# Kernel optimization log

Hardware: AMD Instinct MI355X
Metric: run time of the kernel (lower is better)

Reference implementation:

```python
import jax, jax.numpy as jnp
import numpy as np

N = 100000       # nodes
E = 3200000      # edges (avg degree 32)
NFEAT, NHID, NCLASS = 256, 128, 40


def setup_inputs() -> dict:
    key = jax.random.key(0)
    ks = jax.random.split(key, 6)
    x = jax.random.normal(ks[0], (N, NFEAT), jnp.float32)
    edge_rows = jax.random.randint(ks[1], (E,), 0, N)   # destination nodes
    edge_cols = jax.random.randint(ks[2], (E,), 0, N)   # source nodes
    # SageConv proj: Linear(2*in, out, bias=False); weight stored [out, in] torch-style
    W1 = jax.random.normal(ks[3], (NHID, 2 * NFEAT), jnp.float32) * 0.05
    W2 = jax.random.normal(ks[4], (NHID, 2 * NHID), jnp.float32) * 0.05
    mlp_W = jax.random.normal(ks[5], (NCLASS, NHID), jnp.float32) * 0.05  # init.normal_(std=0.05)
    mlp_b = jnp.zeros((NCLASS,), jnp.float32)
    return {"x": x, "W1": W1, "W2": W2, "mlp_W": mlp_W, "mlp_b": mlp_b,
            "edge_rows": edge_rows, "edge_cols": edge_cols}


def _sage_conv(h, W, rows, cols, deg):
    # neigh = spmm(adj, h) / (deg + 1); adj binary COO (rows <- cols)
    neigh = jax.ops.segment_sum(h[cols], rows, num_segments=N) / (deg + 1.0)[:, None]
    return jnp.concatenate([h, neigh], axis=-1) @ W.T


def reference(x, W1, W2, mlp_W, mlp_b, edge_rows, edge_cols):
    deg = jax.ops.segment_sum(jnp.ones((E,), x.dtype), edge_rows, num_segments=N)
    h = jax.nn.relu(_sage_conv(x, W1, edge_rows, edge_cols, deg))   # dropout: eval no-op
    h = jax.nn.relu(_sage_conv(h, W2, edge_rows, edge_cols, deg))
    logits = h @ mlp_W.T + mlp_b
    return jax.nn.log_softmax(logits, axis=1)
```

## Files before the change

kernel.cpp:

```cpp
#include <hip/hip_runtime.h>
#include <hip/hip_bf16.h>

#define NFEAT 256
#define NHID  128
#define NCLASS 40

typedef __attribute__((ext_vector_type(8))) short short8;
typedef __attribute__((ext_vector_type(4))) float float4v;

__device__ __forceinline__ unsigned short f2bf(float f) {
    union { float f; unsigned u; } v; v.f = f;
    unsigned r = v.u + 0x7fff + ((v.u >> 16) & 1);
    return (unsigned short)(r >> 16);
}
__device__ __forceinline__ float bflo(unsigned u) { return __uint_as_float(u << 16); }
__device__ __forceinline__ float bfhi(unsigned u) { return __uint_as_float(u & 0xffff0000u); }
__device__ __forceinline__ unsigned cvtpk_bf16(float a, float b) {
    unsigned r;
    asm("v_cvt_pk_bf16_f32 %0, %1, %2" : "=v"(r) : "v"(a), "v"(b));
    return r;
}

__device__ __forceinline__ void ld_g2l16(const unsigned short* gp, unsigned short* lp) {
    __builtin_amdgcn_global_load_lds((const __attribute__((address_space(1))) unsigned short*)gp,
                                     (__attribute__((address_space(3))) unsigned short*)lp,
                                     16, 0, 0);
}

#define TILE_E 4096
#define WCAP   20480


__global__ __launch_bounds__(256) void prep_fused(const int* __restrict__ rows,
                                                  const int* __restrict__ cols,
                                                  int* __restrict__ gcur,
                                                  unsigned* __restrict__ binned, int E, int nbuck,
                                                  int nblk,
                                                  const float* __restrict__ W1,
                                                  const float* __restrict__ W2,
                                                  const float* __restrict__ Wm,
                                                  unsigned short* __restrict__ Wp1,
                                                  unsigned short* __restrict__ Wp2,
                                                  unsigned short* __restrict__ Wb,
                                                  const float* __restrict__ X,
                                                  unsigned short* __restrict__ X16, int N) {
    int t = threadIdx.x;
    if ((int)blockIdx.x >= nblk + 560) {
        int idx0 = (blockIdx.x - nblk - 560) * 2048;
        #pragma unroll
        for (int it = 0; it < 8; ++it) {
            int idx = idx0 + it * 256 + t;
            int r = idx >> 5, u = idx & 31;
            if (r < N) {
                const float4* px = reinterpret_cast<const float4*>(X + (size_t)r * 256 + u * 8);
                float4 v0 = px[0], v1 = px[1];
                uint4 q;
                q.x = cvtpk_bf16(v0.x, v0.y); q.y = cvtpk_bf16(v0.z, v0.w);
                q.z = cvtpk_bf16(v1.x, v1.y); q.w = cvtpk_bf16(v1.z, v1.w);
                *reinterpret_cast<uint4*>(&X16[(size_t)r * 256 + ((u ^ (r & 7)) * 8)]) = q;
            }
        }
        return;
    }
    if ((int)blockIdx.x >= nblk) {
        int b = blockIdx.x - nblk;
        if (b < 256) {
            float v = (b < 128) ? W1[b * 512 + t] : W1[(b - 128) * 512 + 256 + t];
            Wp1[(size_t)(t >> 5) * 8192 + b * 32 + (t & 31)] = f2bf(v);
        } else if (b < 512) {
            int o = b - 256;
            if (t < 128) {
                float v = (o < 128) ? W2[o * 256 + t] : W2[(o - 128) * 256 + 128 + t];
                Wp2[(size_t)(t >> 5) * 8192 + o * 32 + (t & 31)] = f2bf(v);
            }
        } else {
            int o = b - 512;
            if (t < 128) Wb[o * 128 + t] = (o < NCLASS) ? f2bf(Wm[o * 128 + t]) : 0;
        }
        return;
    }
    __shared__ int hh[256];
    __shared__ int lbase[256];
    __shared__ int lcur[256];
    hh[t] = 0;
    __syncthreads();
    int e0 = blockIdx.x * TILE_E;
    int4 rv[4];
    #pragma unroll
    for (int it = 0; it < TILE_E / 1024; ++it) {
        int base = e0 + (it * 256 + t) * 4;
        if (base + 3 < E) {
            rv[it] = *reinterpret_cast<const int4*>(&rows[base]);
            atomicAdd(&hh[rv[it].x >> 9], 1);
            atomicAdd(&hh[rv[it].y >> 9], 1);
            atomicAdd(&hh[rv[it].z >> 9], 1);
            atomicAdd(&hh[rv[it].w >> 9], 1);
        } else {
            for (int k = 0; k < 4; ++k)
                if (base + k < E) atomicAdd(&hh[rows[base + k] >> 9], 1);
        }
    }
    __syncthreads();
    if (t < nbuck) {
        int h = hh[t];
        lbase[t] = t * WCAP + (h ? atomicAdd(&gcur[t], h) : 0);
        lcur[t] = 0;
    }
    __syncthreads();
    #pragma unroll
    for (int it = 0; it < TILE_E / 1024; ++it) {
        int base = e0 + (it * 256 + t) * 4;
        if (base + 3 < E) {
            int4 r = rv[it];
            int4 c = *reinterpret_cast<const int4*>(&cols[base]);
            int b0 = r.x >> 9, b1 = r.y >> 9, b2 = r.z >> 9, b3 = r.w >> 9;
            int d0 = lbase[b0] + atomicAdd(&lcur[b0], 1);
            int d1 = lbase[b1] + atomicAdd(&lcur[b1], 1);
            int d2 = lbase[b2] + atomicAdd(&lcur[b2], 1);
            int d3 = lbase[b3] + atomicAdd(&lcur[b3], 1);
            binned[d0] = ((unsigned)(r.x & 511) << 17) | (unsigned)c.x;
            binned[d1] = ((unsigned)(r.y & 511) << 17) | (unsigned)c.y;
            binned[d2] = ((unsigned)(r.z & 511) << 17) | (unsigned)c.z;
            binned[d3] = ((unsigned)(r.w & 511) << 17) | (unsigned)c.w;
        } else {
            for (int k = 0; k < 4; ++k)
                if (base + k < E) {
                    int r = rows[base + k];
                    int b = r >> 9;
                    int dst = lbase[b] + atomicAdd(&lcur[b], 1);
                    binned[dst] = ((unsigned)(r & 511) << 17) | (unsigned)cols[base + k];
                }
        }
    }
}

__global__ __launch_bounds__(512) void gemm1_fw(const unsigned short* __restrict__ X16,
                                                const unsigned short* __restrict__ Wp,
                                                unsigned short* __restrict__ PS,
                                                unsigned char* __restrict__ PN8,
                                                int M, int nfw,
                                                const unsigned* __restrict__ binned,
                                                const int* __restrict__ gcur,
                                                int4* __restrict__ rpd,
                                                int* __restrict__ csr_cols, int N) {
    __shared__ __align__(16) char smem[65536];
    const int t = threadIdx.x;

    if ((int)blockIdx.x < nfw) {
        int* h    = (int*)smem;
        int* ps   = h + 512;
        int* lcur = ps + 256;
        int w = blockIdx.x;
        int r0 = w << 9;
        h[t] = 0;
        if (t < 256) ps[t] = 0;
        __syncthreads();
        int beg = w * WCAP, end = beg + gcur[w];
        for (int e = beg + t; e < end; e += 512)
            atomicAdd(&h[binned[e] >> 17], 1);
        __syncthreads();
        int pair = 0;
        if (t < 256) { pair = h[2 * t] + h[2 * t + 1]; ps[t] = pair; }
        __syncthreads();
        for (int off = 1; off < 256; off <<= 1) {
            int tmp = (t >= off && t < 256) ? ps[t - off] : 0;
            __syncthreads();
            if (t < 256) ps[t] += tmp;
            __syncthreads();
        }
        if (t < 256) {
            int base0 = beg + ps[t] - pair;
            int base1 = base0 + h[2 * t];
            int r_a = r0 + 2 * t, r_b = r0 + 2 * t + 1;
            if (r_a < N) {
                int4 m; m.x = base0; m.y = h[2 * t];
                m.z = __float_as_int(1.0f / ((float)h[2 * t] + 1.0f)); m.w = 0;
                rpd[r_a] = m;
            }
            if (r_b < N) {
                int4 m; m.x = base1; m.y = h[2 * t + 1];
                m.z = __float_as_int(1.0f / ((float)h[2 * t + 1] + 1.0f)); m.w = 0;
                rpd[r_b] = m;
            }
            lcur[2 * t] = base0;
            lcur[2 * t + 1] = base1;
        }
        __syncthreads();
        for (int e = beg + t; e < end; e += 512) {
            unsigned v = binned[e];
            int idx = atomicAdd(&lcur[v >> 17], 1);
            csr_cols[idx] = (int)(v & 0x1FFFFu);
        }
        return;
    }

    unsigned short* const sA = (unsigned short*)smem;
    const int lane = t & 63;
    const int wave = t >> 6;
    const int m0 = (blockIdx.x - nfw) * 128;
    const int wm = (wave >> 2) * 64;
    const int wn = (wave & 3) * 64;
    const int r15 = lane & 15;
    const int l4  = lane >> 4;

    #pragma unroll
    for (int it = 0; it < 8; ++it) {
        int row = it * 16 + (t >> 5);
        int gm  = min(m0 + row, M - 1);
        ld_g2l16(X16 + (size_t)gm * 256 + (t & 31) * 8,
                 (unsigned short*)(smem + it * 8192 + wave * 1024));
    }
    __syncthreads();

    float4v acc[4][4] = {{{0.f,0.f,0.f,0.f}}};
    #pragma unroll
    for (int k = 0; k < 8; ++k) {
        short8 aF[4], bF[4];
        #pragma unroll
        for (int i = 0; i < 4; ++i) {
            int row  = wm + i * 16 + r15;
            int koct = k * 4 + l4;
            int u    = koct ^ (row & 7);
            aF[i] = *reinterpret_cast<const short8*>(&sA[row * 256 + u * 8]);
        }
        #pragma unroll
        for (int j = 0; j < 4; ++j) {
            int o = wn + j * 16 + r15;
            bF[j] = *reinterpret_cast<const short8*>(&Wp[(size_t)k * 8192 + o * 32 + l4 * 8]);
        }
        #pragma unroll
        for (int i = 0; i < 4; ++i)
            #pragma unroll
            for (int j = 0; j < 4; ++j)
                acc[i][j] = __builtin_amdgcn_mfma_f32_16x16x32_bf16(aF[i], bF[j], acc[i][j], 0, 0, 0);
    }

    #pragma unroll
    for (int i = 0; i < 4; ++i) {
        #pragma unroll
        for (int r = 0; r < 4; ++r) {
            int row = m0 + wm + i * 16 + (lane >> 4) * 4 + r;
            #pragma unroll
            for (int j = 0; j < 4; ++j) {
                float v  = acc[i][j][r];
                float vn = __shfl_xor(v, 1);
                int cN = wn + j * 16 + r15;
                if (row < M && !(r15 & 1)) {
                    if (cN < 128) {
                        *reinterpret_cast<unsigned*>(&PS[(size_t)row * 128 + cN]) = cvtpk_bf16(v, vn);
                    } else {
                        unsigned p8 = __builtin_amdgcn_cvt_pk_fp8_f32(v, vn, 0u, false);
                        *reinterpret_cast<unsigned short*>(&PN8[(size_t)row * 128 + (cN - 128)]) =
                            (unsigned short)p8;
                    }
                }
            }
        }
    }
}

__global__ __launch_bounds__(512) void gemm2_mfma(const unsigned short* __restrict__ H,
                                                  const unsigned short* __restrict__ Wp,
                                                  unsigned short* __restrict__ PS,
                                                  unsigned char* __restrict__ PN8,
                                                  int M) {
    __shared__ __align__(16) unsigned short sA[128 * 128];
    const int t    = threadIdx.x;
    const int lane = t & 63;
    const int wave = t >> 6;
    const int m0 = blockIdx.x * 128;
    const int wm = (wave >> 2) * 64;
    const int wn = (wave & 3) * 64;
    const int r15 = lane & 15;
    const int l4  = lane >> 4;

    #pragma unroll
    for (int it = 0; it < 4; ++it) {
        int row = it * 32 + (t >> 4);
        ld_g2l16(H + (size_t)(m0 + row) * 128 + (t & 15) * 8,
                 (unsigned short*)((char*)sA + it * 8192 + wave * 1024));
    }
    __syncthreads();

    float4v acc[4][4] = {{{0.f,0.f,0.f,0.f}}};
    #pragma unroll
    for (int k = 0; k < 4; ++k) {
        short8 aF[4], bF[4];
        #pragma unroll
        for (int i = 0; i < 4; ++i) {
            int row  = wm + i * 16 + r15;
            int koct = k * 4 + l4;
            int u    = koct ^ (row & 7);
            aF[i] = *reinterpret_cast<const short8*>(&sA[row * 128 + u * 8]);
        }
        #pragma unroll
        for (int j = 0; j < 4; ++j) {
            int o = wn + j * 16 + r15;
            bF[j] = *reinterpret_cast<const short8*>(&Wp[(size_t)k * 8192 + o * 32 + l4 * 8]);
        }
        #pragma unroll
        for (int i = 0; i < 4; ++i)
            #pragma unroll
            for (int j = 0; j < 4; ++j)
                acc[i][j] = __builtin_amdgcn_mfma_f32_16x16x32_bf16(aF[i], bF[j], acc[i][j], 0, 0, 0);
    }

    #pragma unroll
    for (int i = 0; i < 4; ++i) {
        #pragma unroll
        for (int r = 0; r < 4; ++r) {
            int row = m0 + wm + i * 16 + (lane >> 4) * 4 + r;
            #pragma unroll
            for (int j = 0; j < 4; ++j) {
                float v  = acc[i][j][r];
                float vn = __shfl_xor(v, 1);
                int cN = wn + j * 16 + r15;
                if (row < M && !(r15 & 1)) {
                    if (cN < 128) {
                        *reinterpret_cast<unsigned*>(&PS[(size_t)row * 128 + cN]) = cvtpk_bf16(v, vn);
                    } else {
                        unsigned p8 = __builtin_amdgcn_cvt_pk_fp8_f32(v, vn, 0u, false);
                        *reinterpret_cast<unsigned short*>(&PN8[(size_t)row * 128 + (cN - 128)]) =
                            (unsigned short)p8;
                    }
                }
            }
        }
    }
}

__device__ __forceinline__ void acc_fp8x8(uint2 u,
                                          float& a0, float& a1, float& a2, float& a3,
                                          float& a4, float& a5, float& a6, float& a7) {
    auto f01 = __builtin_amdgcn_cvt_pk_f32_fp8(u.x, false);
    auto f23 = __builtin_amdgcn_cvt_pk_f32_fp8(u.x, true);
    auto f45 = __builtin_amdgcn_cvt_pk_f32_fp8(u.y, false);
    auto f67 = __builtin_amdgcn_cvt_pk_f32_fp8(u.y, true);
    a0 += f01[0]; a1 += f01[1]; a2 += f23[0]; a3 += f23[1];
    a4 += f45[0]; a5 += f45[1]; a6 += f67[0]; a7 += f67[1];
}

__global__ __launch_bounds__(256) void gather_combine(const unsigned short* __restrict__ PS,
                                                      const unsigned char* __restrict__ PN8,
                                                      const int4* __restrict__ rpd,
                                                      const int* __restrict__ csr_cols,
                                                      unsigned short* __restrict__ H, int N) {
    int node = (blockIdx.x * blockDim.x + threadIdx.x) >> 6;
    if (node >= N) return;
    int lane = threadIdx.x & 63;
    int grp  = lane >> 4;
    int l16  = lane & 15;
    int4 md = rpd[node];
    int beg = md.x, end = md.x + md.y;
    float id = __int_as_float(md.z);

    uint4 us = {0u, 0u, 0u, 0u};
    if (grp == 0)
        us = *reinterpret_cast<const uint4*>(&PS[(size_t)node * 128 + l16 * 8]);

    float a0=0,a1=0,a2=0,a3=0,a4=0,a5=0,a6=0,a7=0;
    int p0 = beg + grp;
    for (; p0 + 12 < end; p0 += 16) {
        int cA = csr_cols[p0];
        int cB = csr_cols[p0 + 4];
        int cC = csr_cols[p0 + 8];
        int cD = csr_cols[p0 + 12];
        uint2 uA = *reinterpret_cast<const uint2*>(&PN8[(size_t)cA * 128 + l16 * 8]);
        uint2 uB = *reinterpret_cast<const uint2*>(&PN8[(size_t)cB * 128 + l16 * 8]);
        uint2 uC = *reinterpret_cast<const uint2*>(&PN8[(size_t)cC * 128 + l16 * 8]);
        uint2 uD = *reinterpret_cast<const uint2*>(&PN8[(size_t)cD * 128 + l16 * 8]);
        acc_fp8x8(uA, a0, a1, a2, a3, a4, a5, a6, a7);
        acc_fp8x8(uB, a0, a1, a2, a3, a4, a5, a6, a7);
        acc_fp8x8(uC, a0, a1, a2, a3, a4, a5, a6, a7);
        acc_fp8x8(uD, a0, a1, a2, a3, a4, a5, a6, a7);
    }
    for (; p0 < end; p0 += 4) {
        int c = csr_cols[p0];
        uint2 u = *reinterpret_cast<const uint2*>(&PN8[(size_t)c * 128 + l16 * 8]);
        acc_fp8x8(u, a0, a1, a2, a3, a4, a5, a6, a7);
    }
    a0 += __shfl_xor(a0, 16); a1 += __shfl_xor(a1, 16);
    a2 += __shfl_xor(a2, 16); a3 += __shfl_xor(a3, 16);
    a4 += __shfl_xor(a4, 16); a5 += __shfl_xor(a5, 16);
    a6 += __shfl_xor(a6, 16); a7 += __shfl_xor(a7, 16);
    a0 += __shfl_xor(a0, 32); a1 += __shfl_xor(a1, 32);
    a2 += __shfl_xor(a2, 32); a3 += __shfl_xor(a3, 32);
    a4 += __shfl_xor(a4, 32); a5 += __shfl_xor(a5, 32);
    a6 += __shfl_xor(a6, 32); a7 += __shfl_xor(a7, 32);

    if (grp == 0) {
        float h0 = fmaxf(fmaf(a0, id, bflo(us.x)), 0.f);
        float h1 = fmaxf(fmaf(a1, id, bfhi(us.x)), 0.f);
        float h2 = fmaxf(fmaf(a2, id, bflo(us.y)), 0.f);
        float h3 = fmaxf(fmaf(a3, id, bfhi(us.y)), 0.f);
        float h4 = fmaxf(fmaf(a4, id, bflo(us.z)), 0.f);
        float h5 = fmaxf(fmaf(a5, id, bfhi(us.z)), 0.f);
        float h6 = fmaxf(fmaf(a6, id, bflo(us.w)), 0.f);
        float h7 = fmaxf(fmaf(a7, id, bfhi(us.w)), 0.f);
        uint4 o;
        o.x = cvtpk_bf16(h0, h1); o.y = cvtpk_bf16(h2, h3);
        o.z = cvtpk_bf16(h4, h5); o.w = cvtpk_bf16(h6, h7);
        *reinterpret_cast<uint4*>(&H[(size_t)node * 128 + ((l16 ^ (node & 7)) * 8)]) = o;
    }
}

__global__ __launch_bounds__(256) void mlp_head_mfma(const unsigned short* __restrict__ H,
                                                     const unsigned short* __restrict__ Wb,
                                                     const float* __restrict__ bm,
                                                     float* __restrict__ out, int N) {
    __shared__ unsigned short sW[48 * 128];
    int t = threadIdx.x;
    for (int i = t; i < 48 * 128 / 2; i += 256)
        ((unsigned*)sW)[i] = ((const unsigned*)Wb)[i];
    __syncthreads();

    const int wave = t >> 6, lane = t & 63;
    const int m0 = blockIdx.x * 64 + wave * 16;
    if (m0 >= N) return;
    const int r15 = lane & 15;
    const int k8  = (lane >> 4) * 8;
    const int arow = min(m0 + r15, N - 1);

    float4v acc[3] = {{0.f,0.f,0.f,0.f},{0.f,0.f,0.f,0.f},{0.f,0.f,0.f,0.f}};
    #pragma unroll
    for (int k0 = 0; k0 < 128; k0 += 32) {
        int u = (k0 >> 3) + (lane >> 4);
        short8 a = *reinterpret_cast<const short8*>(&H[(size_t)arow * 128 + ((u ^ (arow & 7)) * 8)]);
        #pragma unroll
        for (int f = 0; f < 3; ++f) {
            short8 b = *reinterpret_cast<const short8*>(&sW[(f * 16 + r15) * 128 + k0 + k8]);
            acc[f] = __builtin_amdgcn_mfma_f32_16x16x32_bf16(a, b, acc[f], 0, 0, 0);
        }
    }

    float bias[3]; bool cv[3];
    #pragma unroll
    for (int f = 0; f < 3; ++f) {
        int c = f * 16 + r15;
        cv[f] = (c < NCLASS);
        bias[f] = cv[f] ? bm[c] : 0.f;
    }
    #pragma unroll
    for (int r = 0; r < 4; ++r) {
        int node = m0 + (lane >> 4) * 4 + r;
        float lg[3];
        float m = -1e30f;
        #pragma unroll
        for (int f = 0; f < 3; ++f) {
            lg[f] = cv[f] ? (acc[f][r] + bias[f]) : -1e30f;
            m = fmaxf(m, lg[f]);
        }
        m = fmaxf(m, __shfl_xor(m, 1));
        m = fmaxf(m, __shfl_xor(m, 2));
        m = fmaxf(m, __shfl_xor(m, 4));
        m = fmaxf(m, __shfl_xor(m, 8));
        float s = 0.f;
        #pragma unroll
        for (int f = 0; f < 3; ++f) s += cv[f] ? __expf(lg[f] - m) : 0.f;
        s += __shfl_xor(s, 1);
        s += __shfl_xor(s, 2);
        s += __shfl_xor(s, 4);
        s += __shfl_xor(s, 8);
        float ls = __logf(s);
        if (node < N) {
            #pragma unroll
            for (int f = 0; f < 3; ++f)
                if (cv[f]) out[(size_t)node * NCLASS + f * 16 + r15] = lg[f] - m - ls;
        }
    }
}

extern "C" void kernel_launch(void* const* d_in, const int* in_sizes, int n_in,
                              void* d_out, int out_size, void* d_ws, size_t ws_size,
                              hipStream_t stream) {
    const float* x    = (const float*)d_in[0];
    const float* W1   = (const float*)d_in[1];
    const float* W2   = (const float*)d_in[2];
    const float* mlpW = (const float*)d_in[3];
    const float* mlpb = (const float*)d_in[4];
    const int*   rows = (const int*)d_in[5];
    const int*   cols = (const int*)d_in[6];

    const int N = in_sizes[0] / NFEAT;
    const int E = in_sizes[5];

    char* ws = (char*)d_ws;
    size_t off = 0;
    auto alloc = [&](size_t bytes) -> void* {
        void* p = ws + off;
        off = (off + bytes + 255) & ~(size_t)255;
        return p;
    };
    const int nbuck = (N + 511) >> 9;
    const int nblk  = (E + TILE_E - 1) / TILE_E;

    unsigned short* PS  = (unsigned short*)alloc((size_t)N * 128 * 2);
    unsigned char*  PN8 = (unsigned char*) alloc((size_t)N * 128);
    unsigned short* H   = (unsigned short*)alloc((size_t)N * 128 * 2);
    unsigned short* X16 = (unsigned short*)alloc((size_t)N * 256 * 2);
    int4*  RPD    = (int4*) alloc((size_t)N * 16);
    int*   CSRC   = (int*)  alloc((size_t)nbuck * WCAP * 4);
    unsigned* BINNED = (unsigned*)alloc((size_t)nbuck * WCAP * 4);
    int*   GCUR   = (int*)  alloc((size_t)256 * 4);
    unsigned short* Wp1 = (unsigned short*)alloc((size_t)256 * 256 * 2);
    unsigned short* Wp2 = (unsigned short*)alloc((size_t)128 * 256 * 2);
    unsigned short* Wb  = (unsigned short*)alloc((size_t)48 * 128 * 2);

    const int mblocks = (N + 127) / 128;
    const int gblocks = (int)(((long long)N * 64 + 255) / 256);
    const int ncvt    = (N * 32 + 2047) / 2048;

    hipMemsetAsync(GCUR, 0, 256 * 4, stream);
    prep_fused<<<nblk + 560 + ncvt, 256, 0, stream>>>(rows, cols, GCUR, BINNED, E, nbuck, nblk,
                                                      W1, W2, mlpW, Wp1, Wp2, Wb, x, X16, N);

    gemm1_fw<<<nbuck + mblocks, 512, 0, stream>>>(X16, Wp1, PS, PN8, N, nbuck,
                                                  BINNED, GCUR, RPD, CSRC, N);
    gather_combine<<<gblocks, 256, 0, stream>>>(PS, PN8, RPD, CSRC, H, N);

    gemm2_mfma<<<mblocks, 512, 0, stream>>>(H, Wp2, PS, PN8, N);
    gather_combine<<<gblocks, 256, 0, stream>>>(PS, PN8, RPD, CSRC, H, N);

    mlp_head_mfma<<<(N + 63) / 64, 256, 0, stream>>>(H, Wb, mlpb, (float*)d_out, N);
}
```

Before: 431.7 us.

## Fuse X bf16 conversion into gemm1 and second gather into MLP head

The separate pass that converts X from fp32 to bf16 is removed. gemm1 now loads fp32 X directly, converts it in registers and writes the swizzled bf16 tile into LDS. The second gather_combine and the MLP head are merged into one gather_head kernel, which computes each node's hidden vector in registers and applies the 40-class projection and log-softmax with shuffles. This saves the X16 write and read round trip, the H write and read, and one launch. In exchange the head uses scalar dot products instead of MFMA, and gemm1's tile load becomes synchronous register loads instead of direct global-to-LDS.

```diff
diff --git a/kernel.cpp b/kernel.cpp
--- a/kernel.cpp
+++ b/kernel.cpp
@@ -41,27 +41,8 @@
                                                   const float* __restrict__ Wm,
                                                   unsigned short* __restrict__ Wp1,
                                                   unsigned short* __restrict__ Wp2,
-                                                  unsigned short* __restrict__ Wb,
-                                                  const float* __restrict__ X,
-                                                  unsigned short* __restrict__ X16, int N) {
+                                                  unsigned short* __restrict__ Wb) {
     int t = threadIdx.x;
-    if ((int)blockIdx.x >= nblk + 560) {
-        int idx0 = (blockIdx.x - nblk - 560) * 2048;
-        #pragma unroll
-        for (int it = 0; it < 8; ++it) {
-            int idx = idx0 + it * 256 + t;
-            int r = idx >> 5, u = idx & 31;
-            if (r < N) {
-                const float4* px = reinterpret_cast<const float4*>(X + (size_t)r * 256 + u * 8);
-                float4 v0 = px[0], v1 = px[1];
-                uint4 q;
-                q.x = cvtpk_bf16(v0.x, v0.y); q.y = cvtpk_bf16(v0.z, v0.w);
-                q.z = cvtpk_bf16(v1.x, v1.y); q.w = cvtpk_bf16(v1.z, v1.w);
-                *reinterpret_cast<uint4*>(&X16[(size_t)r * 256 + ((u ^ (r & 7)) * 8)]) = q;
-            }
-        }
-        return;
-    }
     if ((int)blockIdx.x >= nblk) {
         int b = blockIdx.x - nblk;
         if (b < 256) {
@@ -134,7 +115,7 @@
     }
 }
 
-__global__ __launch_bounds__(512) void gemm1_fw(const unsigned short* __restrict__ X16,
+__global__ __launch_bounds__(512) void gemm1_fw(const float* __restrict__ X,
                                                 const unsigned short* __restrict__ Wp,
                                                 unsigned short* __restrict__ PS,
                                                 unsigned char* __restrict__ PN8,
@@ -203,12 +184,19 @@
     const int r15 = lane & 15;
     const int l4  = lane >> 4;
 
-    #pragma unroll
-    for (int it = 0; it < 8; ++it) {
-        int row = it * 16 + (t >> 5);
-        int gm  = min(m0 + row, M - 1);
-        ld_g2l16(X16 + (size_t)gm * 256 + (t & 31) * 8,
-                 (unsigned short*)(smem + it * 8192 + wave * 1024));
+    const int ar = t >> 2;
+    const int q4 = t & 3;
+    const int gm = min(m0 + ar, M - 1);
+    const float* gx = X + (size_t)gm * 256 + q4 * 8;
+    #pragma unroll
+    for (int k0 = 0; k0 < 8; ++k0) {
+        float4 v0 = *reinterpret_cast<const float4*>(gx + k0 * 32);
+        float4 v1 = *reinterpret_cast<const float4*>(gx + k0 * 32 + 4);
+        uint4 q;
+        q.x = cvtpk_bf16(v0.x, v0.y); q.y = cvtpk_bf16(v0.z, v0.w);
+        q.z = cvtpk_bf16(v1.x, v1.y); q.w = cvtpk_bf16(v1.z, v1.w);
+        int u = (k0 * 4 + q4) ^ (ar & 7);
+        *reinterpret_cast<uint4*>(&sA[ar * 256 + u * 8]) = q;
     }
     __syncthreads();
 
@@ -404,70 +392,103 @@
     }
 }
 
-__global__ __launch_bounds__(256) void mlp_head_mfma(const unsigned short* __restrict__ H,
-                                                     const unsigned short* __restrict__ Wb,
-                                                     const float* __restrict__ bm,
-                                                     float* __restrict__ out, int N) {
-    __shared__ unsigned short sW[48 * 128];
+__global__ __launch_bounds__(256) void gather_head(const unsigned short* __restrict__ PS,
+                                                   const unsigned char* __restrict__ PN8,
+                                                   const int4* __restrict__ rpd,
+                                                   const int* __restrict__ csr_cols,
+                                                   const unsigned short* __restrict__ Wb,
+                                                   const float* __restrict__ bm,
+                                                   float* __restrict__ out, int N) {
+    __shared__ unsigned short sW[40 * 136];
+    __shared__ float sB[40];
     int t = threadIdx.x;
-    for (int i = t; i < 48 * 128 / 2; i += 256)
-        ((unsigned*)sW)[i] = ((const unsigned*)Wb)[i];
+    for (int i = t; i < 40 * 64; i += 256) {
+        int c = i >> 6, j = i & 63;
+        reinterpret_cast<unsigned*>(&sW[c * 136])[j] =
+            reinterpret_cast<const unsigned*>(&Wb[c * 128])[j];
+    }
+    if (t < 40) sB[t] = bm[t];
     __syncthreads();
 
-    const int wave = t >> 6, lane = t & 63;
-    const int m0 = blockIdx.x * 64 + wave * 16;
-    if (m0 >= N) return;
-    const int r15 = lane & 15;
-    const int k8  = (lane >> 4) * 8;
-    const int arow = min(m0 + r15, N - 1);
-
-    float4v acc[3] = {{0.f,0.f,0.f,0.f},{0.f,0.f,0.f,0.f},{0.f,0.f,0.f,0.f}};
-    #pragma unroll
-    for (int k0 = 0; k0 < 128; k0 += 32) {
-        int u = (k0 >> 3) + (lane >> 4);
-        short8 a = *reinterpret_cast<const short8*>(&H[(size_t)arow * 128 + ((u ^ (arow & 7)) * 8)]);
-        #pragma unroll
-        for (int f = 0; f < 3; ++f) {
-            short8 b = *reinterpret_cast<const short8*>(&sW[(f * 16 + r15) * 128 + k0 + k8]);
-            acc[f] = __builtin_amdgcn_mfma_f32_16x16x32_bf16(a, b, acc[f], 0, 0, 0);
-        }
-    }
-
-    float bias[3]; bool cv[3];
-    #pragma unroll
-    for (int f = 0; f < 3; ++f) {
-        int c = f * 16 + r15;
-        cv[f] = (c < NCLASS);
-        bias[f] = cv[f] ? bm[c] : 0.f;
-    }
-    #pragma unroll
-    for (int r = 0; r < 4; ++r) {
-        int node = m0 + (lane >> 4) * 4 + r;
-        float lg[3];
-        float m = -1e30f;
-        #pragma unroll
-        for (int f = 0; f < 3; ++f) {
-            lg[f] = cv[f] ? (acc[f][r] + bias[f]) : -1e30f;
-            m = fmaxf(m, lg[f]);
-        }
-        m = fmaxf(m, __shfl_xor(m, 1));
-        m = fmaxf(m, __shfl_xor(m, 2));
-        m = fmaxf(m, __shfl_xor(m, 4));
-        m = fmaxf(m, __shfl_xor(m, 8));
-        float s = 0.f;
-        #pragma unroll
-        for (int f = 0; f < 3; ++f) s += cv[f] ? __expf(lg[f] - m) : 0.f;
-        s += __shfl_xor(s, 1);
-        s += __shfl_xor(s, 2);
-        s += __shfl_xor(s, 4);
-        s += __shfl_xor(s, 8);
-        float ls = __logf(s);
-        if (node < N) {
-            #pragma unroll
-            for (int f = 0; f < 3; ++f)
-                if (cv[f]) out[(size_t)node * NCLASS + f * 16 + r15] = lg[f] - m - ls;
-        }
-    }
+    int node = (blockIdx.x * blockDim.x + t) >> 6;
+    if (node >= N) return;
+    int lane = t & 63;
+    int grp  = lane >> 4;
+    int l16  = lane & 15;
+    int4 md = rpd[node];
+    int beg = md.x, end = md.x + md.y;
+    float id = __int_as_float(md.z);
+
+    uint4 us = *reinterpret_cast<const uint4*>(&PS[(size_t)node * 128 + l16 * 8]);
+
+    float a0=0,a1=0,a2=0,a3=0,a4=0,a5=0,a6=0,a7=0;
+    int p0 = beg + grp;
+    for (; p0 + 12 < end; p0 += 16) {
+        int cA = csr_cols[p0];
+        int cB = csr_cols[p0 + 4];
+        int cC = csr_cols[p0 + 8];
+        int cD = csr_cols[p0 + 12];
+        uint2 uA = *reinterpret_cast<const uint2*>(&PN8[(size_t)cA * 128 + l16 * 8]);
+        uint2 uB = *reinterpret_cast<const uint2*>(&PN8[(size_t)cB * 128 + l16 * 8]);
+        uint2 uC = *reinterpret_cast<const uint2*>(&PN8[(size_t)cC * 128 + l16 * 8]);
+        uint2 uD = *reinterpret_cast<const uint2*>(&PN8[(size_t)cD * 128 + l16 * 8]);
+        acc_fp8x8(uA, a0, a1, a2, a3, a4, a5, a6, a7);
+        acc_fp8x8(uB, a0, a1, a2, a3, a4, a5, a6, a7);
+        acc_fp8x8(uC, a0, a1, a2, a3, a4, a5, a6, a7);
+        acc_fp8x8(uD, a0, a1, a2, a3, a4, a5, a6, a7);
+    }
+    for (; p0 < end; p0 += 4) {
+        int c = csr_cols[p0];
+        uint2 u = *reinterpret_cast<const uint2*>(&PN8[(size_t)c * 128 + l16 * 8]);
+        acc_fp8x8(u, a0, a1, a2, a3, a4, a5, a6, a7);
+    }
+    a0 += __shfl_xor(a0, 16); a1 += __shfl_xor(a1, 16);
+    a2 += __shfl_xor(a2, 16); a3 += __shfl_xor(a3, 16);
+    a4 += __shfl_xor(a4, 16); a5 += __shfl_xor(a5, 16);
+    a6 += __shfl_xor(a6, 16); a7 += __shfl_xor(a7, 16);
+    a0 += __shfl_xor(a0, 32); a1 += __shfl_xor(a1, 32);
+    a2 += __shfl_xor(a2, 32); a3 += __shfl_xor(a3, 32);
+    a4 += __shfl_xor(a4, 32); a5 += __shfl_xor(a5, 32);
+    a6 += __shfl_xor(a6, 32); a7 += __shfl_xor(a7, 32);
+
+    float h0 = fmaxf(fmaf(a0, id, bflo(us.x)), 0.f);
+    float h1 = fmaxf(fmaf(a1, id, bfhi(us.x)), 0.f);
+    float h2 = fmaxf(fmaf(a2, id, bflo(us.y)), 0.f);
+    float h3 = fmaxf(fmaf(a3, id, bfhi(us.y)), 0.f);
+    float h4 = fmaxf(fmaf(a4, id, bflo(us.z)), 0.f);
+    float h5 = fmaxf(fmaf(a5, id, bfhi(us.z)), 0.f);
+    float h6 = fmaxf(fmaf(a6, id, bflo(us.w)), 0.f);
+    float h7 = fmaxf(fmaf(a7, id, bfhi(us.w)), 0.f);
+
+    float lg[10];
+    #pragma unroll
+    for (int q = 0; q < 10; ++q) {
+        int c = grp * 10 + q;
+        uint4 wv = *reinterpret_cast<const uint4*>(&sW[c * 136 + l16 * 8]);
+        float p = h0 * bflo(wv.x) + h1 * bfhi(wv.x)
+                + h2 * bflo(wv.y) + h3 * bfhi(wv.y)
+                + h4 * bflo(wv.z) + h5 * bfhi(wv.z)
+                + h6 * bflo(wv.w) + h7 * bfhi(wv.w);
+        p += __shfl_xor(p, 1);
+        p += __shfl_xor(p, 2);
+        p += __shfl_xor(p, 4);
+        p += __shfl_xor(p, 8);
+        lg[q] = p + sB[c];
+    }
+    float m = lg[0];
+    #pragma unroll
+    for (int q = 1; q < 10; ++q) m = fmaxf(m, lg[q]);
+    m = fmaxf(m, __shfl_xor(m, 16));
+    m = fmaxf(m, __shfl_xor(m, 32));
+    float s = 0.f;
+    #pragma unroll
+    for (int q = 0; q < 10; ++q) s += __expf(lg[q] - m);
+    s += __shfl_xor(s, 16);
+    s += __shfl_xor(s, 32);
+    float ls = __logf(s);
+    #pragma unroll
+    for (int q = 0; q < 10; ++q)
+        if (l16 == q) out[(size_t)node * NCLASS + grp * 10 + q] = lg[q] - m - ls;
 }
 
 extern "C" void kernel_launch(void* const* d_in, const int* in_sizes, int n_in,
@@ -497,7 +518,6 @@
     unsigned short* PS  = (unsigned short*)alloc((size_t)N * 128 * 2);
     unsigned char*  PN8 = (unsigned char*) alloc((size_t)N * 128);
     unsigned short* H   = (unsigned short*)alloc((size_t)N * 128 * 2);
-    unsigned short* X16 = (unsigned short*)alloc((size_t)N * 256 * 2);
     int4*  RPD    = (int4*) alloc((size_t)N * 16);
     int*   CSRC   = (int*)  alloc((size_t)nbuck * WCAP * 4);
     unsigned* BINNED = (unsigned*)alloc((size_t)nbuck * WCAP * 4);
@@ -508,18 +528,16 @@
 
     const int mblocks = (N + 127) / 128;
     const int gblocks = (int)(((long long)N * 64 + 255) / 256);
-    const int ncvt    = (N * 32 + 2047) / 2048;
 
     hipMemsetAsync(GCUR, 0, 256 * 4, stream);
-    prep_fused<<<nblk + 560 + ncvt, 256, 0, stream>>>(rows, cols, GCUR, BINNED, E, nbuck, nblk,
-                                                      W1, W2, mlpW, Wp1, Wp2, Wb, x, X16, N);
-
-    gemm1_fw<<<nbuck + mblocks, 512, 0, stream>>>(X16, Wp1, PS, PN8, N, nbuck,
+    prep_fused<<<nblk + 560, 256, 0, stream>>>(rows, cols, GCUR, BINNED, E, nbuck, nblk,
+                                               W1, W2, mlpW, Wp1, Wp2, Wb);
+
+    gemm1_fw<<<nbuck + mblocks, 512, 0, stream>>>(x, Wp1, PS, PN8, N, nbuck,
                                                   BINNED, GCUR, RPD, CSRC, N);
     gather_combine<<<gblocks, 256, 0, stream>>>(PS, PN8, RPD, CSRC, H, N);
 
     gemm2_mfma<<<mblocks, 512, 0, stream>>>(H, Wp2, PS, PN8, N);
-    gather_combine<<<gblocks, 256, 0, stream>>>(PS, PN8, RPD, CSRC, H, N);
-
-    mlp_head_mfma<<<(N + 63) / 64, 256, 0, stream>>>(H, Wb, mlpb, (float*)d_out, N);
-}
+
+    gather_head<<<gblocks, 256, 0, stream>>>(PS, PN8, RPD, CSRC, Wb, mlpb, (float*)d_out, N);
+}
```

After: 471.8 us. 1.09x slower.
